# Kernel optimization log

Measured on AMD Instinct MI355X. Metric: run time of the kernel, lower is better.

The kernel has to match this reference:

```python
import jax, jax.numpy as jnp
import numpy as np

NUM_HEAD = 8
ATTN_DIM = 512
WINDOW_WIDTH = 31
HALF_WIN = WINDOW_WIDTH // 2  # symmetric band half-width
NEG_INF = -1e10


def setup_inputs() -> dict:
    key = jax.random.key(0)
    k0, k1, k2 = jax.random.split(key, 3)
    n, c, w = 4, 512, 2048
    out_dim = 512
    input_ = jax.random.normal(k0, (n, c, 1, w), dtype=jnp.float32)
    mask = jnp.ones((n, w), dtype=jnp.float32)  # 1 = valid key position
    # xavier-uniform-like init for the two linears, zero bias (as in the module)
    lim_in = np.sqrt(6.0 / (c + 3 * ATTN_DIM)).astype(np.float32)
    W_in = jax.random.uniform(k1, (3 * ATTN_DIM, c), jnp.float32, -lim_in, lim_in)
    b_in = jnp.zeros((3 * ATTN_DIM,), jnp.float32)
    lim_fc = np.sqrt(6.0 / (ATTN_DIM + out_dim)).astype(np.float32)
    W_fc = jax.random.uniform(k2, (out_dim, ATTN_DIM), jnp.float32, -lim_fc, lim_fc)
    b_fc = jnp.zeros((out_dim,), jnp.float32)
    return {"input_": input_, "mask": mask, "W_in": W_in, "b_in": b_in,
            "W_fc": W_fc, "b_fc": b_fc}


def reference(input_, mask, W_in, b_in, W_fc, b_fc):
    n, c, h, w = input_.shape  # h == 1
    d = ATTN_DIM // NUM_HEAD
    x = input_.reshape(n, c, w).transpose(0, 2, 1)          # [n, w, c]
    temp = x @ W_in.T + b_in                                # [n, w, 3A]
    temp = temp.transpose(0, 2, 1)                          # [n, 3A, w]
    # channel layout after chunk(num_head) then chunk(3): [h, {q,k,v}, d]
    qkv = temp.reshape(n, NUM_HEAD, 3, d, w)
    q, k, v = qkv[:, :, 0], qkv[:, :, 1], qkv[:, :, 2]      # each [n, H, d, w]
    scale = NUM_HEAD / ATTN_DIM                              # == 1/d_head
    attn = jnp.einsum('nhdi,nhdj->nhij', q, k) * scale       # [n, H, w, w]
    # windowed band mask combined with per-key padding mask (clip_mask/mha_mask)
    idx = jnp.arange(w)
    band = jnp.abs(idx[:, None] - idx[None, :]) <= HALF_WIN  # [w, w]
    valid = band[None, None, :, :] & (mask > 0.5)[:, None, None, :]
    attn = jnp.where(valid, attn, NEG_INF)                   # pre-softmax mask
    attn = jax.nn.softmax(attn, axis=-1)
    attn = jnp.where(valid, attn, 0.0)                       # post-softmax mask
    # dropout in eval mode (identity) for a deterministic reference
    out = jnp.einsum('nhdj,nhij->nhdi', v, attn)             # [n, H, d, w]
    out = out.reshape(n, ATTN_DIM, w).transpose(0, 2, 1)     # [n, w, A]
    out = out @ W_fc.T + b_fc                                # [n, w, out_dim]
    od = out.shape[-1]
    return out.transpose(0, 2, 1).reshape(n, od, 1, w)
```

## Files before the change

### kernel.cpp

```cpp
#include <hip/hip_runtime.h>
#include <hip/hip_bf16.h>
#include <math.h>

#define W_SEQ   2048
#define C_IN    512
#define N_BATCH 4
#define NHEAD   8
#define QKV_CH  1536
#define OUT_CH  512
#define ATTND   512
#define N1_4    (QKV_CH * C_IN / 4)
#define N2_4    (OUT_CH * ATTND / 4)

typedef __attribute__((ext_vector_type(8))) short bf16x8;
typedef __attribute__((ext_vector_type(8))) unsigned short u16x8;
typedef __attribute__((ext_vector_type(4))) float f32x4;

__device__ __forceinline__ void gld16(const void* g, void* l) {
    __builtin_amdgcn_global_load_lds((const __attribute__((address_space(1))) void*)g,
                                     (__attribute__((address_space(3))) void*)l, 16, 0, 0);
}
__device__ __forceinline__ unsigned short f2bf(float f) {
    unsigned u = __float_as_uint(f);
    return (unsigned short)((u + 0x7FFFu + ((u >> 16) & 1u)) >> 16);
}
__device__ __forceinline__ unsigned ld_flag(const unsigned* p) {
    return __hip_atomic_load(p, __ATOMIC_RELAXED, __HIP_MEMORY_SCOPE_AGENT);
}

__device__ __forceinline__ void tree_barrier(unsigned* flg) {
    __syncthreads();
    if (threadIdx.x == 0) {
        __threadfence();
        unsigned* leaf = flg + (blockIdx.x >> 4) * 16;
        unsigned* root = flg + 1024;
        unsigned* rel  = flg + 1040;
        if (atomicAdd(leaf, 1u) == 15u)
            if (atomicAdd(root, 1u) == 63u)
                __hip_atomic_store(rel, 1u, __ATOMIC_RELEASE, __HIP_MEMORY_SCOPE_AGENT);
        while (ld_flag(rel) == 0u) __builtin_amdgcn_s_sleep(2);
        __threadfence();
    }
    __syncthreads();
}

__device__ __forceinline__ void prep_unit(char* sm, int b,
    const float* __restrict__ input, unsigned short* __restrict__ Xh,
    const float* __restrict__ W_in, unsigned short* __restrict__ Winh,
    const float* __restrict__ W_fc, unsigned short* __restrict__ Wfch)
{
    const int t = threadIdx.x;
    float (*ts)[65] = (float(*)[65])sm;
    const int n  = b >> 8, rm = b & 255;
    const int i0 = (rm & 31) * 64, c0 = (rm >> 5) * 64;
    const int tx = t & 63, ty = t >> 6;
    #pragma unroll
    for (int s = 0; s < 16; ++s) {
        const int c = s * 4 + ty;
        ts[c][tx] = input[((size_t)(n * C_IN + c0 + c)) * W_SEQ + i0 + tx];
    }
    __syncthreads();
    const int c8 = t & 7, il = t >> 3;
    #pragma unroll
    for (int s = 0; s < 2; ++s) {
        const int i = il + 32 * s;
        u16x8 hv;
        #pragma unroll
        for (int e = 0; e < 8; ++e) hv[e] = f2bf(ts[c8 * 8 + e][i]);
        *(u16x8*)(&Xh[((size_t)(n * W_SEQ + i0 + i)) * C_IN + c0 + c8 * 8]) = hv;
    }
    const int idx = b * 256 + t;
    if (idx < N1_4) {
        const float4 v = ((const float4*)W_in)[idx];
        ushort4 hh; hh.x = f2bf(v.x); hh.y = f2bf(v.y); hh.z = f2bf(v.z); hh.w = f2bf(v.w);
        ((ushort4*)Winh)[idx] = hh;
    } else {
        const int j = idx - N1_4;
        const float4 v = ((const float4*)W_fc)[j];
        ushort4 hh; hh.x = f2bf(v.x); hh.y = f2bf(v.y); hh.z = f2bf(v.z); hh.w = f2bf(v.w);
        ((ushort4*)Wfch)[j] = hh;
    }
}

template<int EPI>
__device__ __forceinline__ void gemm_body(char* sm, int bx, int by,
    const unsigned short* __restrict__ A, const unsigned short* __restrict__ B,
    const float* __restrict__ bias, void* __restrict__ Cv, const int ldc)
{
    const int t = threadIdx.x;
    const int l = t & 63, w = t >> 6;
    const int m0 = by * 128, n0 = bx * 128;
    const int wm = w >> 1, wn = w & 1;

    const int subrow = l >> 3;
    const int swz    = ((l & 7) ^ subrow) << 4;
    const char* pA = (const char*)A + (size_t)m0 * 1024 + swz;
    const char* pB = (const char*)B + (size_t)n0 * 1024 + swz;

    const int frow = l & 15;
    f32x4 acc[4][4] = {};

    for (int k0 = 0; k0 < 512; k0 += 64) {
        const int kb = k0 * 2;
        #pragma unroll
        for (int c = 0; c < 4; ++c) {
            const int q = 4 * w + c;
            const size_t roff = (size_t)(q * 8 + subrow) * 1024 + kb;
            gld16(pA + roff, sm +         q * 1024);
            gld16(pB + roff, sm + 16384 + q * 1024);
        }
        __syncthreads();
        #pragma unroll
        for (int kk = 0; kk < 2; ++kk) {
            const int cswz = (kk * 64 + ((l >> 4) << 4)) ^ ((l & 7) << 4);
            bf16x8 a[4], b[4];
            #pragma unroll
            for (int mi = 0; mi < 4; ++mi)
                a[mi] = *(const bf16x8*)(sm + (wm * 64 + mi * 16 + frow) * 128 + cswz);
            #pragma unroll
            for (int ni = 0; ni < 4; ++ni)
                b[ni] = *(const bf16x8*)(sm + 16384 + (wn * 64 + ni * 16 + frow) * 128 + cswz);
            #pragma unroll
            for (int mi = 0; mi < 4; ++mi)
                #pragma unroll
                for (int ni = 0; ni < 4; ++ni)
                    acc[mi][ni] = __builtin_amdgcn_mfma_f32_16x16x32_bf16(a[mi], b[ni], acc[mi][ni], 0, 0, 0);
        }
        __syncthreads();
    }

    const int g = l >> 4;
    #pragma unroll
    for (int mi = 0; mi < 4; ++mi) {
        #pragma unroll
        for (int ni = 0; ni < 4; ++ni) {
            const int colg = n0 + wn * 64 + ni * 16 + frow;
            #pragma unroll
            for (int r = 0; r < 4; ++r) {
                const int rowg = m0 + wm * 64 + mi * 16 + g * 4 + r;
                const float v = acc[mi][ni][r];
                if (EPI == 0) {
                    ((unsigned short*)Cv)[(size_t)rowg * ldc + colg] = f2bf(v + bias[colg]);
                } else {
                    const int nb = colg >> 11, ii = colg & (W_SEQ - 1);
                    ((float*)Cv)[((size_t)(nb * OUT_CH + rowg)) * W_SEQ + ii] = v + bias[rowg];
                }
            }
        }
    }
}

#define VT_OFF  13824
#define MSK_OFF 30208

__device__ __forceinline__ void attn_body(char* sm, int blk,
    const unsigned short* __restrict__ qkv, const float* __restrict__ mask,
    unsigned short* __restrict__ aoh)
{
    const int t = threadIdx.x, l = t & 63, w = t >> 6;
    const int i0 = (blk & 31) * 64, h = (blk >> 5) & 7, n = blk >> 8;
    const int lr = l & 15, lg = l >> 4;

    const char* tb = (const char*)qkv + ((size_t)n * W_SEQ * QKV_CH + h * 192) * 2;

    const int r8 = l >> 3, c8 = l & 7;
    #pragma unroll
    for (int it = 0; it < 3; ++it) {
        const int jl = w * 24 + it * 8 + r8;
        const int jg = i0 - 16 + jl;
        bf16x8 kv = {}, vv = {};
        if (jg >= 0 && jg < W_SEQ) {
            const char* rp = tb + (size_t)jg * 3072;
            kv = *(const bf16x8*)(rp + 128 + c8 * 16);
            vv = *(const bf16x8*)(rp + 256 + c8 * 16);
        }
        *(bf16x8*)(sm + jl * 144 + c8 * 16) = kv;
        const int J0 = jl >> 3;
        #pragma unroll
        for (int e = 0; e < 8; ++e) {
            const int d = c8 * 8 + e;
            const int fold = ((d >> 3) ^ d) & 7;
            *(unsigned short*)(sm + VT_OFF + d * 256 + (((J0 ^ fold) << 4) | ((jl & 7) * 2)))
                = (unsigned short)vv[e];
        }
    }
    bf16x8 qh[2];
    {
        const char* qrow = tb + (size_t)(i0 + w * 16 + lr) * 3072 + lg * 16;
        qh[0] = *(const bf16x8*)(qrow);
        qh[1] = *(const bf16x8*)(qrow + 64);
    }
    if (t < 96) {
        const int jg = i0 - 16 + t;
        *(float*)(sm + MSK_OFF + t * 4) = (jg >= 0 && jg < W_SEQ) ? mask[n * W_SEQ + jg] : 0.f;
    }
    __syncthreads();

    f32x4 sacc[6] = {};
    #pragma unroll
    for (int nf = 0; nf < 6; ++nf) {
        #pragma unroll
        for (int kk = 0; kk < 2; ++kk) {
            const bf16x8 kh = *(const bf16x8*)(sm + (nf * 16 + lr) * 144 + kk * 64 + lg * 16);
            sacc[nf] = __builtin_amdgcn_mfma_f32_16x16x32_bf16(qh[kk], kh, sacc[nf], 0, 0, 0);
        }
    }
    __syncthreads();

    float mv[6];
    #pragma unroll
    for (int nf = 0; nf < 6; ++nf)
        mv[nf] = *(const float*)(sm + MSK_OFF + (nf * 16 + lr) * 4);

    #pragma unroll
    for (int r = 0; r < 4; ++r) {
        const int ri = w * 16 + lg * 4 + r;
        float sv[6], mrow = -1.0e30f;
        #pragma unroll
        for (int nf = 0; nf < 6; ++nf) {
            const int jcol = nf * 16 + lr;
            const bool valid = (jcol > ri) && (jcol <= ri + 31) && (mv[nf] > 0.5f);
            const float s = valid ? sacc[nf][r] * 0.015625f : -1.0e30f;
            sv[nf] = s;
            mrow = fmaxf(mrow, s);
        }
        #pragma unroll
        for (int off = 1; off <= 8; off <<= 1) mrow = fmaxf(mrow, __shfl_xor(mrow, off));
        float ls = 0.f;
        #pragma unroll
        for (int nf = 0; nf < 6; ++nf) {
            float pp = __expf(sv[nf] - mrow);
            pp = (sv[nf] > -1.0e29f) ? pp : 0.f;
            sv[nf] = pp;
            ls += pp;
        }
        #pragma unroll
        for (int off = 1; off <= 8; off <<= 1) ls += __shfl_xor(ls, off);
        const float rinv = (ls > 0.f) ? 1.f / ls : 0.f;
        #pragma unroll
        for (int nf = 0; nf < 6; ++nf)
            *(unsigned short*)(sm + ri * 208 + (nf * 16 + lr) * 2) = f2bf(sv[nf] * rinv);
    }

    f32x4 oacc[4] = {};
    #pragma unroll
    for (int ks = 0; ks < 3; ++ks) {
        const bf16x8 pah = *(const bf16x8*)(sm + (w * 16 + lr) * 208 + ks * 64 + lg * 16);
        #pragma unroll
        for (int nf2 = 0; nf2 < 4; ++nf2) {
            const int dd = nf2 * 16 + lr;
            const int fold = ((dd >> 3) ^ dd) & 7;
            const bf16x8 vb = *(const bf16x8*)(sm + VT_OFF + dd * 256 + (((4 * ks + lg) ^ fold) << 4));
            oacc[nf2] = __builtin_amdgcn_mfma_f32_16x16x32_bf16(pah, vb, oacc[nf2], 0, 0, 0);
        }
    }

    #pragma unroll
    for (int nf2 = 0; nf2 < 4; ++nf2) {
        #pragma unroll
        for (int r = 0; r < 4; ++r) {
            const int ri = w * 16 + lg * 4 + r;
            aoh[((size_t)(n * W_SEQ + i0 + ri)) * ATTND + h * 64 + nf2 * 16 + lr] = f2bf(oacc[nf2][r]);
        }
    }
}

__global__ __launch_bounds__(256, 4) void fused_all_k(
    const float* __restrict__ input, const float* __restrict__ mask,
    const float* __restrict__ W_in,  const float* __restrict__ b_in,
    const float* __restrict__ W_fc,  const float* __restrict__ b_fc,
    float* __restrict__ out,
    unsigned short* __restrict__ QKVh, unsigned short* __restrict__ AOh,
    unsigned short* __restrict__ Winh, unsigned short* __restrict__ Wfch,
    unsigned short* __restrict__ Xh, unsigned* __restrict__ flg)
{
    __shared__ __align__(16) char sm[32768];
    const int b = blockIdx.x;
    unsigned* qdone = flg + 2048;
    unsigned* adone = flg + 3072;

    prep_unit(sm, b, input, Xh, W_in, Winh, W_fc, Wfch);
    tree_barrier(flg);

    if (b < 768) {
        const int y8 = b & 7, r = b >> 3;
        const int by = (r / 12) * 8 + y8;
        gemm_body<0>(sm, r % 12, by, Xh, Winh, b_in, QKVh, QKV_CH);
        __syncthreads();
        if (threadIdx.x == 0) {
            __threadfence();
            atomicAdd(qdone + by * 16, 1u);
        }
    }

    {
        const int n = b >> 8, i0 = (b & 31) * 64;
        const int row1 = n * W_SEQ + ((i0 >= 16) ? i0 - 16 : 0);
        const int row2 = n * W_SEQ + ((i0 + 79 <= W_SEQ - 1) ? i0 + 79 : W_SEQ - 1);
        const int t1 = row1 >> 7, t2 = row2 >> 7;
        if (threadIdx.x == 0) {
            while (ld_flag(qdone + t1 * 16) < 12u) __builtin_amdgcn_s_sleep(2);
            while (ld_flag(qdone + t2 * 16) < 12u) __builtin_amdgcn_s_sleep(2);
            __threadfence();
        }
        __syncthreads();
        attn_body(sm, b, QKVh, mask, AOh);
        __syncthreads();
        if (threadIdx.x == 0) {
            __threadfence();
            const int panel = n * 16 + (i0 >> 7);
            atomicAdd(adone + panel * 16, 1u);
        }
    }

    if (b < 256) {
        const int bx = b >> 2, by = b & 3;
        if (threadIdx.x == 0) {
            while (ld_flag(adone + bx * 16) < 16u) __builtin_amdgcn_s_sleep(2);
            __threadfence();
        }
        __syncthreads();
        gemm_body<1>(sm, bx, by, Wfch, AOh, b_fc, out, 0);
    }
}

__global__ __launch_bounds__(256, 4) void prep_sep_k(
    const float* __restrict__ input, unsigned short* __restrict__ Xh,
    const float* __restrict__ W_in, unsigned short* __restrict__ Winh,
    const float* __restrict__ W_fc, unsigned short* __restrict__ Wfch)
{
    __shared__ __align__(16) char sm[32768];
    prep_unit(sm, blockIdx.x, input, Xh, W_in, Winh, W_fc, Wfch);
}
__global__ __launch_bounds__(256, 4) void gemm1_sep_k(
    const unsigned short* __restrict__ A, const unsigned short* __restrict__ B,
    const float* __restrict__ bias, unsigned short* __restrict__ C)
{
    __shared__ __align__(16) char sm[32768];
    const int d = blockIdx.x, y8 = d & 7, r = d >> 3;
    gemm_body<0>(sm, r % 12, (r / 12) * 8 + y8, A, B, bias, C, QKV_CH);
}
__global__ __launch_bounds__(256, 4) void attn_sep_k(
    const unsigned short* __restrict__ qkv, const float* __restrict__ mask,
    unsigned short* __restrict__ aoh)
{
    __shared__ __align__(16) char sm[32768];
    attn_body(sm, blockIdx.x, qkv, mask, aoh);
}
__global__ __launch_bounds__(256, 4) void gemm2_sep_k(
    const unsigned short* __restrict__ A, const unsigned short* __restrict__ B,
    const float* __restrict__ bias, float* __restrict__ out)
{
    __shared__ __align__(16) char sm[32768];
    gemm_body<1>(sm, blockIdx.x >> 2, blockIdx.x & 3, A, B, bias, out, 0);
}

extern "C" void kernel_launch(void* const* d_in, const int* in_sizes, int n_in,
                              void* d_out, int out_size, void* d_ws, size_t ws_size,
                              hipStream_t stream)
{
    const float* input = (const float*)d_in[0];
    const float* mask  = (const float*)d_in[1];
    const float* W_in  = (const float*)d_in[2];
    const float* b_in  = (const float*)d_in[3];
    const float* W_fc  = (const float*)d_in[4];
    const float* b_fc  = (const float*)d_in[5];
    float* out = (float*)d_out;
    char* ws = (char*)d_ws;

    unsigned short* QKVh = (unsigned short*)ws;
    unsigned short* AOh  = (unsigned short*)(ws + 25165824);
    unsigned short* Winh = (unsigned short*)(ws + 33554432);
    unsigned short* Wfch = (unsigned short*)(ws + 35127296);
    unsigned short* Xh   = (unsigned short*)(ws + 35651584);
    unsigned*       flg  = (unsigned*)(ws + 46137344);

    int occ = 0;
    hipOccupancyMaxActiveBlocksPerMultiprocessor(&occ, fused_all_k, 256, 0);

    if (occ >= 4) {
        hipMemsetAsync(flg, 0, 16384, stream);
        fused_all_k<<<dim3(1024), 256, 0, stream>>>(
            input, mask, W_in, b_in, W_fc, b_fc, out,
            QKVh, AOh, Winh, Wfch, Xh, flg);
    } else {
        prep_sep_k <<<dim3(1024), 256, 0, stream>>>(input, Xh, W_in, Winh, W_fc, Wfch);
        gemm1_sep_k<<<dim3(768),  256, 0, stream>>>(Xh, Winh, b_in, QKVh);
        attn_sep_k <<<dim3(1024), 256, 0, stream>>>(QKVh, mask, AOh);
        gemm2_sep_k<<<dim3(256),  256, 0, stream>>>(Wfch, AOh, b_fc, out);
    }
}
```

Baseline: 50.77 us.

## Replace global tree barrier with fine-grained dependency flags and reorder GEMM tiles

Removes the grid-wide barrier after the prep phase. Each block now signals per-panel counters for its X tile, its W_in row panel or W_fc, and the first GEMM waits only on the specific X and weight panels it needs. The first GEMM's row-tile order is rotated so work starts on panels likely ready earlier. The epilogue also hoists bias loads out of the inner loop. This lets phases overlap instead of stalling at a full barrier, at the cost of more atomic counters and spin-waits.

```diff
diff --git a/kernel.cpp b/kernel.cpp
--- a/kernel.cpp
+++ b/kernel.cpp
@@ -28,21 +28,6 @@
     return __hip_atomic_load(p, __ATOMIC_RELAXED, __HIP_MEMORY_SCOPE_AGENT);
 }
 
-__device__ __forceinline__ void tree_barrier(unsigned* flg) {
-    __syncthreads();
-    if (threadIdx.x == 0) {
-        __threadfence();
-        unsigned* leaf = flg + (blockIdx.x >> 4) * 16;
-        unsigned* root = flg + 1024;
-        unsigned* rel  = flg + 1040;
-        if (atomicAdd(leaf, 1u) == 15u)
-            if (atomicAdd(root, 1u) == 63u)
-                __hip_atomic_store(rel, 1u, __ATOMIC_RELEASE, __HIP_MEMORY_SCOPE_AGENT);
-        while (ld_flag(rel) == 0u) __builtin_amdgcn_s_sleep(2);
-        __threadfence();
-    }
-    __syncthreads();
-}
 
 __device__ __forceinline__ void prep_unit(char* sm, int b,
     const float* __restrict__ input, unsigned short* __restrict__ Xh,
@@ -130,20 +115,27 @@
     }
 
     const int g = l >> 4;
+    int cols[4]; float bcol[4];
+    #pragma unroll
+    for (int ni = 0; ni < 4; ++ni) {
+        cols[ni] = n0 + wn * 64 + ni * 16 + frow;
+        bcol[ni] = (EPI == 0) ? bias[cols[ni]] : 0.f;
+    }
     #pragma unroll
     for (int mi = 0; mi < 4; ++mi) {
         #pragma unroll
-        for (int ni = 0; ni < 4; ++ni) {
-            const int colg = n0 + wn * 64 + ni * 16 + frow;
+        for (int r = 0; r < 4; ++r) {
+            const int rowg = m0 + wm * 64 + mi * 16 + g * 4 + r;
+            float brow = 0.f;
+            if (EPI == 1) brow = bias[rowg];
             #pragma unroll
-            for (int r = 0; r < 4; ++r) {
-                const int rowg = m0 + wm * 64 + mi * 16 + g * 4 + r;
+            for (int ni = 0; ni < 4; ++ni) {
                 const float v = acc[mi][ni][r];
                 if (EPI == 0) {
-                    ((unsigned short*)Cv)[(size_t)rowg * ldc + colg] = f2bf(v + bias[colg]);
+                    ((unsigned short*)Cv)[(size_t)rowg * ldc + cols[ni]] = f2bf(v + bcol[ni]);
                 } else {
-                    const int nb = colg >> 11, ii = colg & (W_SEQ - 1);
-                    ((float*)Cv)[((size_t)(nb * OUT_CH + rowg)) * W_SEQ + ii] = v + bias[rowg];
+                    const int nb = cols[ni] >> 11, ii = cols[ni] & (W_SEQ - 1);
+                    ((float*)Cv)[((size_t)(nb * OUT_CH + rowg)) * W_SEQ + ii] = v + brow;
                 }
             }
         }
@@ -276,16 +268,32 @@
 {
     __shared__ __align__(16) char sm[32768];
     const int b = blockIdx.x;
-    unsigned* qdone = flg + 2048;
-    unsigned* adone = flg + 3072;
+    unsigned* xdone  = flg;
+    unsigned* wpanel = flg + 1024;
+    unsigned* wfc    = flg + 1280;
+    unsigned* qdone  = flg + 2048;
+    unsigned* adone  = flg + 3072;
 
     prep_unit(sm, b, input, Xh, W_in, Winh, W_fc, Wfch);
-    tree_barrier(flg);
+    __syncthreads();
+    if (threadIdx.x == 0) {
+        __threadfence();
+        atomicAdd(xdone + ((b >> 8) * 16 + ((b & 31) >> 1)) * 16, 1u);
+        if (b < 768) atomicAdd(wpanel + (b >> 6) * 16, 1u);
+        else         atomicAdd(wfc, 1u);
+    }
 
     if (b < 768) {
         const int y8 = b & 7, r = b >> 3;
-        const int by = (r / 12) * 8 + y8;
-        gemm_body<0>(sm, r % 12, by, Xh, Winh, b_in, QKVh, QKV_CH);
+        const int bx = r % 12;
+        const int by = (((r / 12) + 6) & 7) * 8 + y8;
+        if (threadIdx.x == 0) {
+            while (ld_flag(wpanel + bx * 16) < 64u) __builtin_amdgcn_s_sleep(2);
+            while (ld_flag(xdone  + by * 16) < 16u) __builtin_amdgcn_s_sleep(2);
+            __threadfence();
+        }
+        __syncthreads();
+        gemm_body<0>(sm, bx, by, Xh, Winh, b_in, QKVh, QKV_CH);
         __syncthreads();
         if (threadIdx.x == 0) {
             __threadfence();
@@ -316,6 +324,7 @@
     if (b < 256) {
         const int bx = b >> 2, by = b & 3;
         if (threadIdx.x == 0) {
+            while (ld_flag(wfc) < 256u) __builtin_amdgcn_s_sleep(2);
             while (ld_flag(adone + bx * 16) < 16u) __builtin_amdgcn_s_sleep(2);
             __threadfence();
         }
@@ -338,7 +347,7 @@
 {
     __shared__ __align__(16) char sm[32768];
     const int d = blockIdx.x, y8 = d & 7, r = d >> 3;
-    gemm_body<0>(sm, r % 12, (r / 12) * 8 + y8, A, B, bias, C, QKV_CH);
+    gemm_body<0>(sm, r % 12, (((r / 12) + 6) & 7) * 8 + y8, A, B, bias, C, QKV_CH);
 }
 __global__ __launch_bounds__(256, 4) void attn_sep_k(
     const unsigned short* __restrict__ qkv, const float* __restrict__ mask,
```

Result: no change. 50.60 us (-0.3%).
